# Optimization experiments

Measured on AMD Instinct MI355X. Metric: run time of the kernel, lower is better.

Reference implementation:

```python
import jax, jax.numpy as jnp
import numpy as np

N0, N1, N2 = 100000, 20000, 4000   # src(block0), dst(block0)=src(block1), dst(block1)
R = 3                               # number of relations
E0, E1 = 160000, 64000              # edges per relation per block
IN_FEATS, HID = 128, 128
TSS, RS = 64, 64
NTOT = 200000                       # global node count for tss/rs embed tables
F_IN = HID + TSS + RS               # IGConv input feature dim = 256


def _lin(key, fi, fo):
    k1, k2 = jax.random.split(key)
    s = float(1.0 / np.sqrt(fi))
    w = jax.random.uniform(k1, (fi, fo), minval=-s, maxval=s, dtype=jnp.float32)
    b = jax.random.uniform(k2, (fo,), minval=-s, maxval=s, dtype=jnp.float32)
    return w, b


def setup_inputs() -> dict:
    ks = jax.random.split(jax.random.key(0), 32)
    inp = {}
    inp["x_user"] = jax.random.normal(ks[0], (N0, IN_FEATS), dtype=jnp.float32)
    inp["tss_embed"] = jax.random.normal(ks[1], (NTOT, TSS), dtype=jnp.float32)
    inp["rs_embed"] = jax.random.normal(ks[2], (NTOT, RS), dtype=jnp.float32)
    inp["src_nid0"] = jax.random.randint(ks[3], (N0,), 0, NTOT)
    inp["src_nid1"] = jax.random.randint(ks[4], (N1,), 0, NTOT)
    inp["e0_src"] = jax.random.randint(ks[5], (R, E0), 0, N0)
    inp["e0_dst"] = jax.random.randint(ks[6], (R, E0), 0, N1)
    inp["e1_src"] = jax.random.randint(ks[7], (R, E1), 0, N1)
    inp["e1_dst"] = jax.random.randint(ks[8], (R, E1), 0, N2)
    inp["embed_w"], inp["embed_b"] = _lin(ks[9], IN_FEATS, HID)
    i = 10
    for l in (1, 2):
        for nm, fi in (("fc1", F_IN), ("fc2", 3 * F_IN), ("fc3", 2 * HID)):
            pw, pb = zip(*[_lin(jax.random.fold_in(ks[i], r), fi, HID) for r in range(R)])
            inp["l%d_%s_w" % (l, nm)] = jnp.stack(pw)  # [R, fi, HID]
            inp["l%d_%s_b" % (l, nm)] = jnp.stack(pb)  # [R, HID]
            i += 1
    inp["attn_w1"], inp["attn_b1"] = _lin(ks[i], HID, HID)
    inp["attn_w2"] = _lin(ks[i + 1], HID, 1)[0]  # Linear(hid,1,bias=False)
    inp["pred_w"], inp["pred_b"] = _lin(ks[i + 2], HID, 1)
    return inp


def _igconv(src_feat, dst_feat, esrc, edst, n_dst, fc1w, fc1b, fc2w, fc2b, fc3w, fc3b):
    # copy_u gather then max/mean/sum segment reductions over destination nodes
    m = src_feat[esrc]                                   # [E, F]
    s = jax.ops.segment_sum(m, edst, num_segments=n_dst)
    deg = jax.ops.segment_sum(jnp.ones(esrc.shape, m.dtype), edst, num_segments=n_dst)
    mean = s / jnp.maximum(deg, 1.0)[:, None]
    mx = jax.ops.segment_max(m, edst, num_segments=n_dst)
    mx = jnp.where(deg[:, None] > 0, mx, jnp.zeros_like(mx))  # DGL zeros for isolated dst
    msg = jnp.concatenate([mx, mean, s], axis=1)         # [n_dst, 3F]
    inp = jnp.concatenate([msg @ fc2w + fc2b, dst_feat @ fc1w + fc1b], axis=1)
    return jax.nn.relu(inp) @ fc3w + fc3b                # [n_dst, HID]


def _attn(z, w1, b1, w2):
    # SemanticAttention: z [N, R, HID]
    w = (jnp.tanh(z @ w1 + b1) @ w2).mean(0)             # [R, 1]
    beta = jax.nn.softmax(w, axis=0)                     # [R, 1]
    return (beta[None] * z).sum(1)                       # [N, HID]


def _forward(x_user, tss_embed, rs_embed, embed_w, embed_b,
             l1_fc1_w, l1_fc1_b, l1_fc2_w, l1_fc2_b, l1_fc3_w, l1_fc3_b,
             l2_fc1_w, l2_fc1_b, l2_fc2_w, l2_fc2_b, l2_fc3_w, l2_fc3_b,
             attn_w1, attn_b1, attn_w2, pred_w, pred_b,
             src_nid0, src_nid1, e0_src, e0_dst, e1_src, e1_dst):
    u0 = x_user @ embed_w + embed_b                      # self.embed
    feat0 = jnp.concatenate([u0, tss_embed[src_nid0], rs_embed[src_nid0]], axis=1)  # [N0,256]
    conv1 = jax.vmap(lambda es, ed, w1, b1, w2, b2, w3, b3:
                     _igconv(feat0, feat0[:N1], es, ed, N1, w1, b1, w2, b2, w3, b3))
    z1 = conv1(e0_src, e0_dst, l1_fc1_w, l1_fc1_b, l1_fc2_w, l1_fc2_b, l1_fc3_w, l1_fc3_b)  # [R,N1,HID]
    h1 = jax.nn.relu(_attn(jnp.transpose(z1, (1, 0, 2)), attn_w1, attn_b1, attn_w2))  # [N1,HID]
    feat1 = jnp.concatenate([h1, tss_embed[src_nid1], rs_embed[src_nid1]], axis=1)    # [N1,256]
    conv2 = jax.vmap(lambda es, ed, w1, b1, w2, b2, w3, b3:
                     _igconv(feat1, feat1[:N2], es, ed, N2, w1, b1, w2, b2, w3, b3))
    z2 = conv2(e1_src, e1_dst, l2_fc1_w, l2_fc1_b, l2_fc2_w, l2_fc2_b, l2_fc3_w, l2_fc3_b)  # [R,N2,HID]
    h2 = _attn(jnp.transpose(z2, (1, 0, 2)), attn_w1, attn_b1, attn_w2)              # [N2,HID]
    return jax.nn.sigmoid(h2 @ pred_w + pred_b)          # [N2,1]


def reference(x_user, tss_embed, rs_embed, src_nid0, src_nid1,
              e0_src, e0_dst, e1_src, e1_dst, embed_w, embed_b,
              l1_fc1_w, l1_fc1_b, l1_fc2_w, l1_fc2_b, l1_fc3_w, l1_fc3_b,
              l2_fc1_w, l2_fc1_b, l2_fc2_w, l2_fc2_b, l2_fc3_w, l2_fc3_b,
              attn_w1, attn_b1, attn_w2, pred_w, pred_b):
    return _forward(x_user, tss_embed, rs_embed, embed_w, embed_b,
                    l1_fc1_w, l1_fc1_b, l1_fc2_w, l1_fc2_b, l1_fc3_w, l1_fc3_b,
                    l2_fc1_w, l2_fc1_b, l2_fc2_w, l2_fc2_b, l2_fc3_w, l2_fc3_b,
                    attn_w1, attn_b1, attn_w2, pred_w, pred_b,
                    src_nid0, src_nid1, e0_src, e0_dst, e1_src, e1_dst)
```

## Files before the change

kernel.cpp:

```cpp
#include <hip/hip_runtime.h>
#include <math.h>


typedef short s16x8 __attribute__((ext_vector_type(8)));
typedef float f32x4 __attribute__((ext_vector_type(4)));

__device__ __forceinline__ ushort f2bf(float f) {
  unsigned u = __float_as_uint(f);
  return (ushort)((u + 0x7FFFu + ((u >> 16) & 1u)) >> 16);
}
__device__ __forceinline__ float bf2f(unsigned hbits) {
  return __uint_as_float(hbits << 16);
}
__device__ __forceinline__ unsigned pack2(float lo, float hi) {
  return (unsigned)f2bf(lo) | ((unsigned)f2bf(hi) << 16);
}

struct PrepAll {
  const float* src[8];
  ushort* dst[8];
  int K[8];
  int total[8];
};

__global__ __launch_bounds__(256) void prep_all(PrepAll P)
{
  int t = blockIdx.z;
  int off = blockIdx.x * 256 + threadIdx.x;
  if (off >= P.total[t]) return;
  int K = P.K[t];
  int k = off % K;
  int n = (off / K) & 127;
  int r = off / (K * 128);
  P.dst[t][off] = f2bf(P.src[t][((size_t)r * K + k) * 128 + n]);
}

struct GemmDesc {
  const void* A; int lda; size_t aStride; int aKind;
  const ushort* Wt; size_t wStride;
  const float* bias; int biasStride;
  void* C; int ldc; size_t cStride; int cKind;
  int M, K, relu;
  const ushort* aggM; const ushort* aggS; const float* invdeg;
  size_t aggStride; int invStride;
  const int* gnid; const float* gtss; const float* grs;
};

template<int AKIND>
__device__ __forceinline__ uint4 loadA(const void* Ab, const ushort* AgM,
                                       const ushort* AgS, int lda, int row,
                                       bool rowOK, int k0, int quad, float idg)
{
  uint4 pk = make_uint4(0u, 0u, 0u, 0u);
  if (rowOK) {
    if constexpr (AKIND == 1) {
      pk = *(const uint4*)((const ushort*)Ab + (size_t)row * lda + k0 + quad * 8);
    } else if constexpr (AKIND == 0) {
      const float* A32 = (const float*)Ab;
      float4 fa = *(const float4*)(A32 + (size_t)row * lda + k0 + quad * 8);
      float4 fb = *(const float4*)(A32 + (size_t)row * lda + k0 + quad * 8 + 4);
      pk.x = pack2(fa.x, fa.y); pk.y = pack2(fa.z, fa.w);
      pk.z = pack2(fb.x, fb.y); pk.w = pack2(fb.z, fb.w);
    } else {
      int seg = k0 >> 8;
      int jj  = (k0 & 255) + quad * 8;
      const ushort* Ag = (seg == 0) ? AgM : AgS;
      pk = *(const uint4*)(Ag + (size_t)row * 256 + jj);
      if (seg == 1) {
        pk.x = pack2(bf2f(pk.x & 0xFFFFu) * idg, bf2f(pk.x >> 16) * idg);
        pk.y = pack2(bf2f(pk.y & 0xFFFFu) * idg, bf2f(pk.y >> 16) * idg);
        pk.z = pack2(bf2f(pk.z & 0xFFFFu) * idg, bf2f(pk.z >> 16) * idg);
        pk.w = pack2(bf2f(pk.w & 0xFFFFu) * idg, bf2f(pk.w >> 16) * idg);
      }
    }
  }
  return pk;
}

template<int K, int AKIND>
__device__ __forceinline__ void gemm_core(const GemmDesc& d, int r, ushort* Bs)
{
  constexpr int NC = K / 64;
  constexpr int NF = K / 32;

  const int tid = threadIdx.x;
  const int wave = tid >> 6, lane = tid & 63;
  const int m16 = lane & 15, quad = lane >> 4;
  const int rowBase = blockIdx.x * 64;
  const int row = rowBase + wave * 16 + m16;
  const bool rowOK = row < d.M;
  const ushort* Wt = d.Wt + (size_t)r * d.wStride;

  const void* Ab = (const char*)d.A +
      (size_t)r * d.aStride * (AKIND == 0 ? sizeof(float) : sizeof(ushort));
  const ushort* AgM = d.aggM + (size_t)r * d.aggStride;
  const ushort* AgS = d.aggS + (size_t)r * d.aggStride;

  float idg = 1.f;
  if (AKIND == 2 && rowOK) idg = d.invdeg[(size_t)r * d.invStride + row];

  f32x4 acc[8];
  #pragma unroll
  for (int j = 0; j < 8; ++j)
    #pragma unroll
    for (int p = 0; p < 4; ++p) acc[j][p] = 0.f;

  uint4 pkAll[(K <= 256) ? NF : 2];
  if constexpr (K <= 256) {
    #pragma unroll
    for (int f = 0; f < NF; ++f)
      pkAll[f] = loadA<AKIND>(Ab, AgM, AgS, d.lda, row, rowOK, f * 32, quad, idg);
  }

  #pragma unroll
  for (int c = 0; c < NC; ++c) {
    if constexpr (K > 256) {
      pkAll[0] = loadA<AKIND>(Ab, AgM, AgS, d.lda, row, rowOK, c * 64,      quad, idg);
      pkAll[1] = loadA<AKIND>(Ab, AgM, AgS, d.lda, row, rowOK, c * 64 + 32, quad, idg);
    }
    if (c) __syncthreads();
    #pragma unroll
    for (int i = 0; i < 4; ++i) {
      int q = tid + 256 * i;
      int col = ((q >> 6) & 7) * 16 + (q & 15);
      int kk  = c * 64 + ((q >> 9) & 1) * 32 + ((q >> 4) & 3) * 8;
      *(uint4*)&Bs[q * 8] = *(const uint4*)(Wt + (size_t)col * K + kk);
    }
    __syncthreads();

    #pragma unroll
    for (int ks = 0; ks < 2; ++ks) {
      uint4 pk = (K <= 256) ? pkAll[c * 2 + ks] : pkAll[ks];
      s16x8 af = *(s16x8*)&pk;
      #pragma unroll
      for (int j = 0; j < 8; ++j) {
        s16x8 bf = *(const s16x8*)&Bs[((ks * 8 + j) * 64 + lane) * 8];
        acc[j] = __builtin_amdgcn_mfma_f32_16x16x32_bf16(af, bf, acc[j], 0, 0, 0);
      }
    }
  }

  const float* bias = d.bias + (size_t)r * d.biasStride;
  float bcol[8];
  #pragma unroll
  for (int j = 0; j < 8; ++j) bcol[j] = bias[j * 16 + m16];

  #pragma unroll
  for (int p = 0; p < 4; ++p) {
    int grow = rowBase + wave * 16 + quad * 4 + p;
    if (grow >= d.M) continue;
    if (d.cKind == 0) {
      float* Crow = (float*)d.C + (size_t)r * d.cStride + (size_t)grow * d.ldc;
      #pragma unroll
      for (int j = 0; j < 8; ++j) {
        float v = acc[j][p] + bcol[j];
        if (d.relu) v = fmaxf(v, 0.f);
        Crow[j * 16 + m16] = v;
      }
    } else {
      ushort* Crow = (ushort*)d.C + (size_t)r * d.cStride + (size_t)grow * d.ldc;
      #pragma unroll
      for (int j = 0; j < 8; ++j) {
        float v = acc[j][p] + bcol[j];
        if (d.relu) v = fmaxf(v, 0.f);
        Crow[j * 16 + m16] = f2bf(v);
      }
    }
  }

  if constexpr (K == 128) {
    if (d.gnid) {
      #pragma unroll
      for (int i = 0; i < 8; ++i) {
        int q = tid + 256 * i;
        int grow = rowBase + (q >> 5);
        int c = q & 31;
        if (grow >= d.M) continue;
        int id = d.gnid[grow];
        float4 v = (c < 16) ? *(const float4*)(d.gtss + (size_t)id * 64 + c * 4)
                            : *(const float4*)(d.grs  + (size_t)id * 64 + (c - 16) * 4);
        uint2 g; g.x = pack2(v.x, v.y); g.y = pack2(v.z, v.w);
        *(uint2*)((ushort*)d.C + (size_t)grow * d.ldc + 128 + c * 4) = g;
      }
    }
  }
}

__global__ __launch_bounds__(256, 4) void gemm_mfma(GemmDesc d0, GemmDesc d1)
{
  __shared__ __align__(16) ushort Bs[1024 * 8];
  const GemmDesc& d = blockIdx.z ? d1 : d0;
  const int r = blockIdx.y;
  if (d.K == 128)      gemm_core<128, 0>(d, r, Bs);
  else if (d.K == 256) gemm_core<256, 1>(d, r, Bs);
  else                 gemm_core<768, 2>(d, r, Bs);
}

__global__ __launch_bounds__(256) void fc3_attn(
    const ushort* __restrict__ inp, size_t aStride,
    const ushort* __restrict__ wt3, size_t wStride,
    const float* __restrict__ b3,
    float* __restrict__ z, size_t zStride, int M,
    const ushort* __restrict__ w1t, const float* __restrict__ b1,
    const float* __restrict__ w2, float* __restrict__ wsum)
{
  __shared__ __align__(16) ushort Zs[64 * 128];
  __shared__ __align__(16) ushort Ws[1024 * 8];

  const int tid = threadIdx.x;
  const int wave = tid >> 6, lane = tid & 63;
  const int m16 = lane & 15, quad = lane >> 4;
  const int r = blockIdx.y;
  const int rowBase = blockIdx.x * 64;
  const int row = rowBase + wave * 16 + m16;
  const bool rowOK = row < M;

  const ushort* A  = inp + (size_t)r * aStride;
  const ushort* Wt = wt3 + (size_t)r * wStride;

  f32x4 acc[8];
  #pragma unroll
  for (int j = 0; j < 8; ++j)
    #pragma unroll
    for (int p = 0; p < 4; ++p) acc[j][p] = 0.f;

  uint4 pkAll[8];
  #pragma unroll
  for (int f = 0; f < 8; ++f) {
    uint4 pk = make_uint4(0u, 0u, 0u, 0u);
    if (rowOK) pk = *(const uint4*)(A + (size_t)row * 256 + f * 32 + quad * 8);
    pkAll[f] = pk;
  }

  #pragma unroll
  for (int c = 0; c < 4; ++c) {
    if (c) __syncthreads();
    #pragma unroll
    for (int i = 0; i < 4; ++i) {
      int q = tid + 256 * i;
      int col = ((q >> 6) & 7) * 16 + (q & 15);
      int kk  = c * 64 + ((q >> 9) & 1) * 32 + ((q >> 4) & 3) * 8;
      *(uint4*)&Ws[q * 8] = *(const uint4*)(Wt + (size_t)col * 256 + kk);
    }
    __syncthreads();
    #pragma unroll
    for (int ks = 0; ks < 2; ++ks) {
      s16x8 af = *(s16x8*)&pkAll[c * 2 + ks];
      #pragma unroll
      for (int j = 0; j < 8; ++j) {
        s16x8 bf = *(const s16x8*)&Ws[((ks * 8 + j) * 64 + lane) * 8];
        acc[j] = __builtin_amdgcn_mfma_f32_16x16x32_bf16(af, bf, acc[j], 0, 0, 0);
      }
    }
  }

  const float* bias = b3 + (size_t)r * 128;
  float bcol[8];
  #pragma unroll
  for (int j = 0; j < 8; ++j) bcol[j] = bias[j * 16 + m16];

  #pragma unroll
  for (int p = 0; p < 4; ++p) {
    int lrow = wave * 16 + quad * 4 + p;
    int grow = rowBase + lrow;
    bool ok = grow < M;
    float* Zr = z + (size_t)r * zStride + (size_t)grow * 128;
    #pragma unroll
    for (int j = 0; j < 8; ++j) {
      float v = ok ? acc[j][p] + bcol[j] : 0.f;
      if (ok) Zr[j * 16 + m16] = v;
      int byte = lrow * 256 + (j * 16 + m16) * 2;
      byte ^= (lrow & 7) << 4;
      *(ushort*)((char*)Zs + byte) = f2bf(v);
    }
  }

  f32x4 acc2[8];
  #pragma unroll
  for (int j = 0; j < 8; ++j)
    #pragma unroll
    for (int p = 0; p < 4; ++p) acc2[j][p] = 0.f;

  const int arow = wave * 16 + m16;
  #pragma unroll
  for (int c = 0; c < 2; ++c) {
    __syncthreads();
    #pragma unroll
    for (int i = 0; i < 4; ++i) {
      int q = tid + 256 * i;
      int col = ((q >> 6) & 7) * 16 + (q & 15);
      int kk  = c * 64 + ((q >> 9) & 1) * 32 + ((q >> 4) & 3) * 8;
      *(uint4*)&Ws[q * 8] = *(const uint4*)(w1t + (size_t)col * 128 + kk);
    }
    __syncthreads();
    #pragma unroll
    for (int ks = 0; ks < 2; ++ks) {
      int kk = c * 64 + ks * 32 + quad * 8;
      int byte = arow * 256 + kk * 2;
      byte ^= (arow & 7) << 4;
      s16x8 af = *(const s16x8*)((const char*)Zs + byte);
      #pragma unroll
      for (int j = 0; j < 8; ++j) {
        s16x8 bf = *(const s16x8*)&Ws[((ks * 8 + j) * 64 + lane) * 8];
        acc2[j] = __builtin_amdgcn_mfma_f32_16x16x32_bf16(af, bf, acc2[j], 0, 0, 0);
      }
    }
  }

  float b1c[8], w2c[8];
  #pragma unroll
  for (int j = 0; j < 8; ++j) { b1c[j] = b1[j * 16 + m16]; w2c[j] = w2[j * 16 + m16]; }

  float local = 0.f;
  #pragma unroll
  for (int p = 0; p < 4; ++p) {
    int grow = rowBase + wave * 16 + quad * 4 + p;
    if (grow >= M) continue;
    #pragma unroll
    for (int j = 0; j < 8; ++j)
      local += tanhf(acc2[j][p] + b1c[j]) * w2c[j];
  }
  #pragma unroll
  for (int o = 32; o > 0; o >>= 1) local += __shfl_down(local, o);
  __shared__ float red[4];
  if (lane == 0) red[wave] = local;
  __syncthreads();
  if (tid == 0) atomicAdd(&wsum[r], red[0] + red[1] + red[2] + red[3]);
}

struct Csr6 {
  const int* edst0; const int* edst1;
  const int* esrc0; const int* esrc1;
  int E0, E1, N1, N2;
  int* deg;
  int* rowptr;
  int* csr;
};

__global__ void count_deg6(Csr6 c)
{
  int y = blockIdx.y, l = y / 3, r = y - l * 3;
  int E = l ? c.E1 : c.E0, N = l ? c.N2 : c.N1;
  const int* ed = l ? c.edst1 : c.edst0;
  int* deg = c.deg + (l ? 3 * c.N1 : 0) + r * N;
  int e = blockIdx.x * 256 + threadIdx.x;
  if (e < E) atomicAdd(&deg[ed[(size_t)r * E + e]], 1);
}

__global__ __launch_bounds__(1024) void scan_kernel6(Csr6 c)
{
  int y = blockIdx.y, l = y / 3, r = y - l * 3;
  int N = l ? c.N2 : c.N1;
  int* dgm = c.deg + (l ? 3 * c.N1 : 0) + r * N;
  int* rp  = c.rowptr + (l ? 3 * (c.N1 + 1) : 0) + r * (N + 1);

  __shared__ int wtot[16];
  __shared__ int chunk_total_s;
  const int tid = threadIdx.x, lane = tid & 63, wid = tid >> 6;
  int running = 0;
  for (int base = 0; base < N; base += 4096) {
    int i0 = base + tid * 4;
    int d0 = 0, d1 = 0, d2 = 0, d3 = 0;
    if (i0 < N) {
      if (i0 + 3 < N) { int4 t = *(const int4*)(dgm + i0); d0 = t.x; d1 = t.y; d2 = t.z; d3 = t.w; }
      else { d0 = dgm[i0]; if (i0+1 < N) d1 = dgm[i0+1]; if (i0+2 < N) d2 = dgm[i0+2]; }
    }
    int tsum = d0 + d1 + d2 + d3;
    int incl = tsum;
    #pragma unroll
    for (int o = 1; o < 64; o <<= 1) {
      int t = __shfl_up(incl, o);
      if (lane >= o) incl += t;
    }
    if (lane == 63) wtot[wid] = incl;
    __syncthreads();
    if (wid == 0 && lane < 16) {
      int t = wtot[lane];
      int inc = t;
      #pragma unroll
      for (int o = 1; o < 16; o <<= 1) {
        int u = __shfl_up(inc, o);
        if (lane >= o) inc += u;
      }
      wtot[lane] = inc - t;
      if (lane == 15) chunk_total_s = inc;
    }
    __syncthreads();
    int excl = running + wtot[wid] + (incl - tsum);
    if (i0 < N) {
      int e1 = excl + d0, e2 = e1 + d1, e3 = e2 + d2;
      if (i0 + 3 < N) {
        *(int4*)(rp + i0) = make_int4(excl, e1, e2, e3);
        *(int4*)(dgm + i0) = make_int4(0, 0, 0, 0);
      } else {
        rp[i0] = excl; dgm[i0] = 0;
        if (i0+1 < N) { rp[i0+1] = e1; dgm[i0+1] = 0; }
        if (i0+2 < N) { rp[i0+2] = e2; dgm[i0+2] = 0; }
      }
    }
    running += chunk_total_s;
    __syncthreads();
  }
  if (tid == 0) rp[N] = running;
}

__global__ void fill_csr6(Csr6 c)
{
  int y = blockIdx.y, l = y / 3, r = y - l * 3;
  int E = l ? c.E1 : c.E0, N = l ? c.N2 : c.N1;
  const int* ed = l ? c.edst1 : c.edst0;
  const int* es = l ? c.esrc1 : c.esrc0;
  int* cur = c.deg + (l ? 3 * c.N1 : 0) + r * N;
  const int* rp = c.rowptr + (l ? 3 * (c.N1 + 1) : 0) + r * (N + 1);
  int* csr = c.csr + (l ? 3 * c.E0 : 0) + (size_t)r * E;
  int e = blockIdx.x * 256 + threadIdx.x;
  if (e >= E) return;
  int dn = ed[(size_t)r * E + e];
  int pos = atomicAdd(&cur[dn], 1);
  csr[rp[dn] + pos] = es[(size_t)r * E + e];
}

__global__ __launch_bounds__(256) void agg_kernel(
    const ushort* __restrict__ feat, const int* __restrict__ csr,
    const int* __restrict__ rowptr, int N, int c0, int cr, int CH, int E,
    ushort* __restrict__ aggS, ushort* __restrict__ aggM, float* __restrict__ invdeg)
{
  const int wid = threadIdx.x >> 6, lane = threadIdx.x & 63;
  const int node = blockIdx.x * 4 + wid;
  if (node >= cr) return;
  const size_t rp = (size_t)blockIdx.y * (N + 1) + c0 + node;
  const int o = blockIdx.y * CH + node;
  const int start = rowptr[rp], end = rowptr[rp + 1];
  const int* ecsr = csr + (size_t)blockIdx.y * E;
  const int j = lane * 4;
  float s0 = 0.f, s1 = 0.f, s2 = 0.f, s3 = 0.f;
  float m0 = -INFINITY, m1 = -INFINITY, m2 = -INFINITY, m3 = -INFINITY;
  int e = start;
  for (; e + 4 <= end; e += 4) {
    int sa = ecsr[e], sb = ecsr[e+1], sc = ecsr[e+2], sd = ecsr[e+3];
    uint2 va = *(const uint2*)(feat + (size_t)sa * 256 + j);
    uint2 vb = *(const uint2*)(feat + (size_t)sb * 256 + j);
    uint2 vc = *(const uint2*)(feat + (size_t)sc * 256 + j);
    uint2 vd = *(const uint2*)(feat + (size_t)sd * 256 + j);
    float a0, a1, a2, a3;
    a0 = bf2f(va.x & 0xFFFFu); a1 = bf2f(va.x >> 16); a2 = bf2f(va.y & 0xFFFFu); a3 = bf2f(va.y >> 16);
    s0 += a0; s1 += a1; s2 += a2; s3 += a3;
    m0 = fmaxf(m0, a0); m1 = fmaxf(m1, a1); m2 = fmaxf(m2, a2); m3 = fmaxf(m3, a3);
    a0 = bf2f(vb.x & 0xFFFFu); a1 = bf2f(vb.x >> 16); a2 = bf2f(vb.y & 0xFFFFu); a3 = bf2f(vb.y >> 16);
    s0 += a0; s1 += a1; s2 += a2; s3 += a3;
    m0 = fmaxf(m0, a0); m1 = fmaxf(m1, a1); m2 = fmaxf(m2, a2); m3 = fmaxf(m3, a3);
    a0 = bf2f(vc.x & 0xFFFFu); a1 = bf2f(vc.x >> 16); a2 = bf2f(vc.y & 0xFFFFu); a3 = bf2f(vc.y >> 16);
    s0 += a0; s1 += a1; s2 += a2; s3 += a3;
    m0 = fmaxf(m0, a0); m1 = fmaxf(m1, a1); m2 = fmaxf(m2, a2); m3 = fmaxf(m3, a3);
    a0 = bf2f(vd.x & 0xFFFFu); a1 = bf2f(vd.x >> 16); a2 = bf2f(vd.y & 0xFFFFu); a3 = bf2f(vd.y >> 16);
    s0 += a0; s1 += a1; s2 += a2; s3 += a3;
    m0 = fmaxf(m0, a0); m1 = fmaxf(m1, a1); m2 = fmaxf(m2, a2); m3 = fmaxf(m3, a3);
  }
  for (; e < end; ++e) {
    int src = ecsr[e];
    uint2 v = *(const uint2*)(feat + (size_t)src * 256 + j);
    float a0 = bf2f(v.x & 0xFFFFu), a1 = bf2f(v.x >> 16);
    float a2 = bf2f(v.y & 0xFFFFu), a3 = bf2f(v.y >> 16);
    s0 += a0; s1 += a1; s2 += a2; s3 += a3;
    m0 = fmaxf(m0, a0); m1 = fmaxf(m1, a1); m2 = fmaxf(m2, a2); m3 = fmaxf(m3, a3);
  }
  if (end == start) { m0 = m1 = m2 = m3 = 0.f; }
  uint2 ps; ps.x = pack2(s0, s1); ps.y = pack2(s2, s3);
  *(uint2*)(aggS + (size_t)o * 256 + j) = ps;
  uint2 pm; pm.x = pack2(m0, m1); pm.y = pack2(m2, m3);
  *(uint2*)(aggM + (size_t)o * 256 + j) = pm;
  if (lane == 0) invdeg[o] = 1.f / fmaxf((float)(end - start), 1.f);
}

__device__ __forceinline__ void beta_from_wsum(const float* wsum, float invN,
                                               float& b0, float& b1, float& b2)
{
  float w0 = wsum[0] * invN, w1 = wsum[1] * invN, w2 = wsum[2] * invN;
  float m  = fmaxf(w0, fmaxf(w1, w2));
  float e0 = expf(w0 - m), e1 = expf(w1 - m), e2 = expf(w2 - m);
  float s  = 1.f / (e0 + e1 + e2);
  b0 = e0 * s; b1 = e1 * s; b2 = e2 * s;
}

__global__ __launch_bounds__(256) void combine1_kernel(
    const float* __restrict__ z1, const float* __restrict__ wsum, float invN,
    const float* __restrict__ tss, const float* __restrict__ rs,
    const int* __restrict__ nid, int N, ushort* __restrict__ feat1)
{
  int n = blockIdx.x * 8 + (threadIdx.x >> 5);
  int c = threadIdx.x & 31;
  if (n >= N) return;
  float b0, b1, b2;
  beta_from_wsum(wsum, invN, b0, b1, b2);
  size_t NH = (size_t)N * 128;
  const float* zp = z1 + (size_t)n * 128 + c * 4;
  float4 v0 = *(const float4*)zp;
  float4 v1 = *(const float4*)(zp + NH);
  float4 v2 = *(const float4*)(zp + 2 * NH);
  float wx = fmaxf(b0 * v0.x + b1 * v1.x + b2 * v2.x, 0.f);
  float wy = fmaxf(b0 * v0.y + b1 * v1.y + b2 * v2.y, 0.f);
  float wz = fmaxf(b0 * v0.z + b1 * v1.z + b2 * v2.z, 0.f);
  float ww = fmaxf(b0 * v0.w + b1 * v1.w + b2 * v2.w, 0.f);
  uint2 g; g.x = pack2(wx, wy); g.y = pack2(wz, ww);
  *(uint2*)(feat1 + (size_t)n * 256 + c * 4) = g;
  int id = nid[n];
  float4 t = (c < 16) ? *(const float4*)(tss + (size_t)id * 64 + c * 4)
                      : *(const float4*)(rs  + (size_t)id * 64 + (c - 16) * 4);
  uint2 g2; g2.x = pack2(t.x, t.y); g2.y = pack2(t.z, t.w);
  *(uint2*)(feat1 + (size_t)n * 256 + 128 + c * 4) = g2;
}

__global__ __launch_bounds__(256) void combine2_pred(
    const float* __restrict__ z2, const float* __restrict__ wsum, float invN,
    int N, const float* __restrict__ pw, const float* __restrict__ pb,
    float* __restrict__ out)
{
  int n = blockIdx.x * 8 + (threadIdx.x >> 5);
  int c = threadIdx.x & 31;
  bool ok = n < N;
  float p = 0.f;
  if (ok) {
    float b0, b1, b2;
    beta_from_wsum(wsum, invN, b0, b1, b2);
    size_t NH = (size_t)N * 128;
    const float* zp = z2 + (size_t)n * 128 + c * 4;
    float4 v0 = *(const float4*)zp;
    float4 v1 = *(const float4*)(zp + NH);
    float4 v2 = *(const float4*)(zp + 2 * NH);
    float4 w = *(const float4*)(pw + c * 4);
    p  = (b0 * v0.x + b1 * v1.x + b2 * v2.x) * w.x;
    p += (b0 * v0.y + b1 * v1.y + b2 * v2.y) * w.y;
    p += (b0 * v0.z + b1 * v1.z + b2 * v2.z) * w.z;
    p += (b0 * v0.w + b1 * v1.w + b2 * v2.w) * w.w;
  }
  #pragma unroll
  for (int o = 16; o > 0; o >>= 1) p += __shfl_down(p, o, 32);
  if (ok && c == 0) out[n] = 1.f / (1.f + expf(-(p + pb[0])));
}

extern "C" void kernel_launch(void* const* d_in, const int* in_sizes, int n_in,
                              void* d_out, int out_size, void* d_ws, size_t ws_size,
                              hipStream_t stream)
{
  const float* x_user  = (const float*)d_in[0];
  const float* tss     = (const float*)d_in[1];
  const float* rs      = (const float*)d_in[2];
  const int* src_nid0  = (const int*)d_in[3];
  const int* src_nid1  = (const int*)d_in[4];
  const int* e0_src    = (const int*)d_in[5];
  const int* e0_dst    = (const int*)d_in[6];
  const int* e1_src    = (const int*)d_in[7];
  const int* e1_dst    = (const int*)d_in[8];
  const float* embed_w = (const float*)d_in[9];
  const float* embed_b = (const float*)d_in[10];
  const float* l1w[3]  = {(const float*)d_in[11], (const float*)d_in[13], (const float*)d_in[15]};
  const float* l1b[3]  = {(const float*)d_in[12], (const float*)d_in[14], (const float*)d_in[16]};
  const float* l2w[3]  = {(const float*)d_in[17], (const float*)d_in[19], (const float*)d_in[21]};
  const float* l2b[3]  = {(const float*)d_in[18], (const float*)d_in[20], (const float*)d_in[22]};
  const float* attn_w1 = (const float*)d_in[23];
  const float* attn_b1 = (const float*)d_in[24];
  const float* attn_w2 = (const float*)d_in[25];
  const float* pred_w  = (const float*)d_in[26];
  const float* pred_b  = (const float*)d_in[27];
  float* out = (float*)d_out;

  const int N0 = in_sizes[0] / 128;
  const int N1 = in_sizes[4];
  const int N2 = out_size;
  const int E0 = in_sizes[5] / 3;
  const int E1 = in_sizes[7] / 3;

  char* wp = (char*)d_ws;
  auto walloc = [&](size_t bytes) {
    char* p = wp; wp += (bytes + 255) & ~(size_t)255; return p;
  };
  ushort* feat0  = (ushort*)walloc((size_t)N0 * 256 * 2);
  ushort* inp    = (ushort*)walloc((size_t)3 * N1 * 256 * 2);
  float*  z      = (float*)walloc((size_t)3 * N1 * 128 * 4);
  ushort* wt_emb = (ushort*)walloc((size_t)128 * 128 * 2);
  ushort* wt_attn = (ushort*)walloc((size_t)128 * 128 * 2);
  ushort* wt_fc1[2], *wt_fc2[2], *wt_fc3[2];
  for (int l = 0; l < 2; ++l) {
    wt_fc1[l] = (ushort*)walloc((size_t)3 * 256 * 128 * 2);
    wt_fc2[l] = (ushort*)walloc((size_t)3 * 768 * 128 * 2);
    wt_fc3[l] = (ushort*)walloc((size_t)3 * 256 * 128 * 2);
  }
  size_t degBytes = ((size_t)3 * (N1 + N2) * 4 + 255) & ~(size_t)255;
  int*   degcnt = (int*)walloc(degBytes);
  float* small  = (float*)walloc(256);
  int*   rowptr = (int*)walloc((size_t)(3 * (N1 + 1) + 3 * (N2 + 1)) * 4);
  int*   csr    = (int*)walloc((size_t)3 * (E0 + E1) * 4);
  float* wsum = small;
  ushort* feat1 = feat0;

  size_t used = (size_t)(wp - (char*)d_ws);
  size_t avail = (ws_size > used + 65536) ? (ws_size - used - 65536) : 0;
  const size_t per_row = (size_t)3 * (2 * 256 * 2 + 4 + 64);
  int CH = (int)(avail / per_row);
  if (CH > N1) CH = N1;
  if (CH < 1024) CH = 1024;
  ushort* aggS   = (ushort*)walloc((size_t)3 * CH * 256 * 2);
  ushort* aggM   = (ushort*)walloc((size_t)3 * CH * 256 * 2);
  float*  invdeg = (float*)walloc((size_t)3 * CH * 4);
  (void)n_in;

  hipMemsetAsync(degcnt, 0, degBytes + 256, stream);

  {
    PrepAll P;
    P.src[0] = embed_w;  P.dst[0] = wt_emb;    P.K[0] = 128; P.total[0] = 128 * 128;
    P.src[1] = attn_w1;  P.dst[1] = wt_attn;   P.K[1] = 128; P.total[1] = 128 * 128;
    P.src[2] = l1w[0];   P.dst[2] = wt_fc1[0]; P.K[2] = 256; P.total[2] = 3 * 256 * 128;
    P.src[3] = l1w[1];   P.dst[3] = wt_fc2[0]; P.K[3] = 768; P.total[3] = 3 * 768 * 128;
    P.src[4] = l1w[2];   P.dst[4] = wt_fc3[0]; P.K[4] = 256; P.total[4] = 3 * 256 * 128;
    P.src[5] = l2w[0];   P.dst[5] = wt_fc1[1]; P.K[5] = 256; P.total[5] = 3 * 256 * 128;
    P.src[6] = l2w[1];   P.dst[6] = wt_fc2[1]; P.K[6] = 768; P.total[6] = 3 * 768 * 128;
    P.src[7] = l2w[2];   P.dst[7] = wt_fc3[1]; P.K[7] = 256; P.total[7] = 3 * 256 * 128;
    prep_all<<<dim3((3 * 768 * 128 + 255) / 256, 1, 8), 256, 0, stream>>>(P);
  }

  GemmDesc dz = {};
  dz.K = 256;

  {
    GemmDesc d{};
    d.A = x_user; d.lda = 128; d.aStride = 0; d.aKind = 0;
    d.Wt = wt_emb; d.wStride = 0; d.bias = embed_b; d.biasStride = 0;
    d.C = feat0; d.ldc = 256; d.cStride = 0; d.cKind = 1;
    d.M = N0; d.K = 128; d.relu = 0;
    d.aggM = aggM; d.aggS = aggS; d.invdeg = invdeg; d.aggStride = 0; d.invStride = 0;
    d.gnid = src_nid0; d.gtss = tss; d.grs = rs;
    gemm_mfma<<<dim3((N0 + 63) / 64, 1, 1), 256, 0, stream>>>(d, dz);
  }

  Csr6 c6;
  c6.edst0 = e0_dst; c6.edst1 = e1_dst;
  c6.esrc0 = e0_src; c6.esrc1 = e1_src;
  c6.E0 = E0; c6.E1 = E1; c6.N1 = N1; c6.N2 = N2;
  c6.deg = degcnt; c6.rowptr = rowptr; c6.csr = csr;
  {
    int Emax = E0 > E1 ? E0 : E1;
    count_deg6<<<dim3((Emax + 255) / 256, 6), 256, 0, stream>>>(c6);
    scan_kernel6<<<dim3(1, 6), 1024, 0, stream>>>(c6);
    fill_csr6<<<dim3((Emax + 255) / 256, 6), 256, 0, stream>>>(c6);
  }

  for (int layer = 0; layer < 2; ++layer) {
    const ushort* featS = layer ? feat1 : feat0;
    int Nd = layer ? N2 : N1;
    int E  = layer ? E1 : E0;
    const float* const* lb = layer ? l2b : l1b;
    const int* rp_l  = rowptr + (layer ? 3 * (N1 + 1) : 0);
    const int* csr_l = csr + (layer ? 3 * E0 : 0);
    float* wsum_l = wsum + 3 * layer;

    for (int c0 = 0; c0 < Nd; c0 += CH) {
      int cr = (Nd - c0 < CH) ? (Nd - c0) : CH;
      agg_kernel<<<dim3((cr + 3) / 4, 3), 256, 0, stream>>>(
          featS, csr_l, rp_l, Nd, c0, cr, CH, E, aggS, aggM, invdeg);
      GemmDesc d2{};
      d2.A = nullptr; d2.lda = 0; d2.aStride = 0; d2.aKind = 2;
      d2.Wt = wt_fc2[layer]; d2.wStride = (size_t)768 * 128; d2.bias = lb[1]; d2.biasStride = 128;
      d2.C = inp + (size_t)c0 * 256; d2.ldc = 256; d2.cStride = (size_t)Nd * 256; d2.cKind = 1;
      d2.M = cr; d2.K = 768; d2.relu = 1;
      d2.aggM = aggM; d2.aggS = aggS; d2.invdeg = invdeg;
      d2.aggStride = (size_t)CH * 256; d2.invStride = CH;
      GemmDesc d1{};
      d1.A = featS + (size_t)c0 * 256; d1.lda = 256; d1.aStride = 0; d1.aKind = 1;
      d1.Wt = wt_fc1[layer]; d1.wStride = (size_t)256 * 128; d1.bias = lb[0]; d1.biasStride = 128;
      d1.C = inp + 128 + (size_t)c0 * 256; d1.ldc = 256; d1.cStride = (size_t)Nd * 256; d1.cKind = 1;
      d1.M = cr; d1.K = 256; d1.relu = 1;
      d1.aggM = aggM; d1.aggS = aggS; d1.invdeg = invdeg; d1.aggStride = 0; d1.invStride = 0;
      gemm_mfma<<<dim3((cr + 63) / 64, 3, 2), 256, 0, stream>>>(d2, d1);
    }

    fc3_attn<<<dim3((Nd + 63) / 64, 3), 256, 0, stream>>>(
        inp, (size_t)Nd * 256, wt_fc3[layer], (size_t)256 * 128, lb[2],
        z, (size_t)Nd * 128, Nd, wt_attn, attn_b1, attn_w2, wsum_l);

    if (layer == 0) {
      combine1_kernel<<<(N1 + 7) / 8, 256, 0, stream>>>(
          z, wsum_l, 1.0f / (float)N1, tss, rs, src_nid1, N1, feat1);
    } else {
      combine2_pred<<<(N2 + 7) / 8, 256, 0, stream>>>(
          z, wsum_l, 1.0f / (float)N2, N2, pred_w, pred_b, out);
    }
  }
}
```

Before: 497.8 us.

## Specialize embed GEMM kernel with LDS-staged coalesced stores and alias z buffer

Moves the K=128 embedding GEMM out of the generic gemm_mfma template into a dedicated embed_mfma kernel. The new kernel stages results through shared memory so each row is written back with full 16-byte stores instead of scattered 2-byte writes, and it fills in the tss/rs gather itself. It also drops the K=128 path from gemm_mfma, which may lower register pressure there. Separately, the z buffer now reuses the unused tail of feat0 when that tail is large enough, which frees workspace and lets the aggregation chunk size grow. The aliasing depends on feat0 rows beyond N1 no longer being needed by the time z is written.

```diff
diff --git a/kernel.cpp b/kernel.cpp
--- a/kernel.cpp
+++ b/kernel.cpp
@@ -35,6 +35,98 @@
   P.dst[t][off] = f2bf(P.src[t][((size_t)r * K + k) * 128 + n]);
 }
 
+__global__ __launch_bounds__(256) void embed_mfma(
+    const float* __restrict__ A, const ushort* __restrict__ Wt,
+    const float* __restrict__ bias, ushort* __restrict__ C, int M,
+    const int* __restrict__ gnid, const float* __restrict__ gtss,
+    const float* __restrict__ grs)
+{
+  __shared__ __align__(16) ushort Bs[1024 * 8];
+  __shared__ __align__(16) ushort Cs[64 * 128];
+
+  const int tid = threadIdx.x;
+  const int wave = tid >> 6, lane = tid & 63;
+  const int m16 = lane & 15, quad = lane >> 4;
+  const int rowBase = blockIdx.x * 64;
+  const int row = rowBase + wave * 16 + m16;
+  const bool rowOK = row < M;
+
+  f32x4 acc[8];
+  #pragma unroll
+  for (int j = 0; j < 8; ++j)
+    #pragma unroll
+    for (int p = 0; p < 4; ++p) acc[j][p] = 0.f;
+
+  uint4 pkAll[4];
+  #pragma unroll
+  for (int f = 0; f < 4; ++f) {
+    uint4 pk = make_uint4(0u, 0u, 0u, 0u);
+    if (rowOK) {
+      float4 fa = *(const float4*)(A + (size_t)row * 128 + f * 32 + quad * 8);
+      float4 fb = *(const float4*)(A + (size_t)row * 128 + f * 32 + quad * 8 + 4);
+      pk.x = pack2(fa.x, fa.y); pk.y = pack2(fa.z, fa.w);
+      pk.z = pack2(fb.x, fb.y); pk.w = pack2(fb.z, fb.w);
+    }
+    pkAll[f] = pk;
+  }
+
+  #pragma unroll
+  for (int c = 0; c < 2; ++c) {
+    if (c) __syncthreads();
+    #pragma unroll
+    for (int i = 0; i < 4; ++i) {
+      int q = tid + 256 * i;
+      int col = ((q >> 6) & 7) * 16 + (q & 15);
+      int kk  = c * 64 + ((q >> 9) & 1) * 32 + ((q >> 4) & 3) * 8;
+      *(uint4*)&Bs[q * 8] = *(const uint4*)(Wt + (size_t)col * 128 + kk);
+    }
+    __syncthreads();
+    #pragma unroll
+    for (int ks = 0; ks < 2; ++ks) {
+      s16x8 af = *(s16x8*)&pkAll[c * 2 + ks];
+      #pragma unroll
+      for (int j = 0; j < 8; ++j) {
+        s16x8 bf = *(const s16x8*)&Bs[((ks * 8 + j) * 64 + lane) * 8];
+        acc[j] = __builtin_amdgcn_mfma_f32_16x16x32_bf16(af, bf, acc[j], 0, 0, 0);
+      }
+    }
+  }
+
+  float bcol[8];
+  #pragma unroll
+  for (int j = 0; j < 8; ++j) bcol[j] = bias[j * 16 + m16];
+
+  #pragma unroll
+  for (int p = 0; p < 4; ++p) {
+    int lrow = wave * 16 + quad * 4 + p;
+    #pragma unroll
+    for (int j = 0; j < 8; ++j)
+      Cs[lrow * 128 + j * 16 + m16] = f2bf(acc[j][p] + bcol[j]);
+  }
+  __syncthreads();
+
+  #pragma unroll
+  for (int i = 0; i < 4; ++i) {
+    int q = tid + 256 * i;
+    int grow = rowBase + (q >> 4);
+    if (grow < M)
+      *(uint4*)(C + (size_t)grow * 256 + (q & 15) * 8) = *(const uint4*)&Cs[q * 8];
+  }
+
+  #pragma unroll
+  for (int i = 0; i < 8; ++i) {
+    int q = tid + 256 * i;
+    int grow = rowBase + (q >> 5);
+    int c = q & 31;
+    if (grow >= M) continue;
+    int id = gnid[grow];
+    float4 v = (c < 16) ? *(const float4*)(gtss + (size_t)id * 64 + c * 4)
+                        : *(const float4*)(grs  + (size_t)id * 64 + (c - 16) * 4);
+    uint2 g; g.x = pack2(v.x, v.y); g.y = pack2(v.z, v.w);
+    *(uint2*)(C + (size_t)grow * 256 + 128 + c * 4) = g;
+  }
+}
+
 struct GemmDesc {
   const void* A; int lda; size_t aStride; int aKind;
   const ushort* Wt; size_t wStride;
@@ -43,7 +135,6 @@
   int M, K, relu;
   const ushort* aggM; const ushort* aggS; const float* invdeg;
   size_t aggStride; int invStride;
-  const int* gnid; const float* gtss; const float* grs;
 };
 
 template<int AKIND>
@@ -55,12 +146,6 @@
   if (rowOK) {
     if constexpr (AKIND == 1) {
       pk = *(const uint4*)((const ushort*)Ab + (size_t)row * lda + k0 + quad * 8);
-    } else if constexpr (AKIND == 0) {
-      const float* A32 = (const float*)Ab;
-      float4 fa = *(const float4*)(A32 + (size_t)row * lda + k0 + quad * 8);
-      float4 fb = *(const float4*)(A32 + (size_t)row * lda + k0 + quad * 8 + 4);
-      pk.x = pack2(fa.x, fa.y); pk.y = pack2(fa.z, fa.w);
-      pk.z = pack2(fb.x, fb.y); pk.w = pack2(fb.z, fb.w);
     } else {
       int seg = k0 >> 8;
       int jj  = (k0 & 255) + quad * 8;
@@ -91,8 +176,7 @@
   const bool rowOK = row < d.M;
   const ushort* Wt = d.Wt + (size_t)r * d.wStride;
 
-  const void* Ab = (const char*)d.A +
-      (size_t)r * d.aStride * (AKIND == 0 ? sizeof(float) : sizeof(ushort));
+  const void* Ab = (const char*)d.A + (size_t)r * d.aStride * sizeof(ushort);
   const ushort* AgM = d.aggM + (size_t)r * d.aggStride;
   const ushort* AgS = d.aggS + (size_t)r * d.aggStride;
 
@@ -167,23 +251,6 @@
       }
     }
   }
-
-  if constexpr (K == 128) {
-    if (d.gnid) {
-      #pragma unroll
-      for (int i = 0; i < 8; ++i) {
-        int q = tid + 256 * i;
-        int grow = rowBase + (q >> 5);
-        int c = q & 31;
-        if (grow >= d.M) continue;
-        int id = d.gnid[grow];
-        float4 v = (c < 16) ? *(const float4*)(d.gtss + (size_t)id * 64 + c * 4)
-                            : *(const float4*)(d.grs  + (size_t)id * 64 + (c - 16) * 4);
-        uint2 g; g.x = pack2(v.x, v.y); g.y = pack2(v.z, v.w);
-        *(uint2*)((ushort*)d.C + (size_t)grow * d.ldc + 128 + c * 4) = g;
-      }
-    }
-  }
 }
 
 __global__ __launch_bounds__(256, 4) void gemm_mfma(GemmDesc d0, GemmDesc d1)
@@ -191,8 +258,7 @@
   __shared__ __align__(16) ushort Bs[1024 * 8];
   const GemmDesc& d = blockIdx.z ? d1 : d0;
   const int r = blockIdx.y;
-  if (d.K == 128)      gemm_core<128, 0>(d, r, Bs);
-  else if (d.K == 256) gemm_core<256, 1>(d, r, Bs);
+  if (d.K == 256)      gemm_core<256, 1>(d, r, Bs);
   else                 gemm_core<768, 2>(d, r, Bs);
 }
 
@@ -576,7 +642,6 @@
   };
   ushort* feat0  = (ushort*)walloc((size_t)N0 * 256 * 2);
   ushort* inp    = (ushort*)walloc((size_t)3 * N1 * 256 * 2);
-  float*  z      = (float*)walloc((size_t)3 * N1 * 128 * 4);
   ushort* wt_emb = (ushort*)walloc((size_t)128 * 128 * 2);
   ushort* wt_attn = (ushort*)walloc((size_t)128 * 128 * 2);
   ushort* wt_fc1[2], *wt_fc2[2], *wt_fc3[2];
@@ -593,9 +658,17 @@
   float* wsum = small;
   ushort* feat1 = feat0;
 
+  size_t zBytes   = (size_t)3 * ((N1 > N2) ? N1 : N2) * 128 * 4;
+  size_t tailBytes = (N0 > N1) ? ((size_t)(N0 - N1) * 512) : 0;
+  float* z;
+  if (tailBytes >= zBytes)
+    z = (float*)((char*)feat0 + (size_t)N1 * 512);
+  else
+    z = (float*)walloc(zBytes);
+
   size_t used = (size_t)(wp - (char*)d_ws);
   size_t avail = (ws_size > used + 65536) ? (ws_size - used - 65536) : 0;
-  const size_t per_row = (size_t)3 * (2 * 256 * 2 + 4 + 64);
+  const size_t per_row = (size_t)3 * (2 * 256 * 2 + 4);
   int CH = (int)(avail / per_row);
   if (CH > N1) CH = N1;
   if (CH < 1024) CH = 1024;
@@ -619,19 +692,8 @@
     prep_all<<<dim3((3 * 768 * 128 + 255) / 256, 1, 8), 256, 0, stream>>>(P);
   }
 
-  GemmDesc dz = {};
-  dz.K = 256;
-
-  {
-    GemmDesc d{};
-    d.A = x_user; d.lda = 128; d.aStride = 0; d.aKind = 0;
-    d.Wt = wt_emb; d.wStride = 0; d.bias = embed_b; d.biasStride = 0;
-    d.C = feat0; d.ldc = 256; d.cStride = 0; d.cKind = 1;
-    d.M = N0; d.K = 128; d.relu = 0;
-    d.aggM = aggM; d.aggS = aggS; d.invdeg = invdeg; d.aggStride = 0; d.invStride = 0;
-    d.gnid = src_nid0; d.gtss = tss; d.grs = rs;
-    gemm_mfma<<<dim3((N0 + 63) / 64, 1, 1), 256, 0, stream>>>(d, dz);
-  }
+  embed_mfma<<<dim3((N0 + 63) / 64), 256, 0, stream>>>(
+      x_user, wt_emb, embed_b, feat0, N0, src_nid0, tss, rs);
 
   Csr6 c6;
   c6.edst0 = e0_dst; c6.edst1 = e1_dst;
```

Result: faster. 486.9 us (-2.2%).
